# Kernel optimization log

Measured on AMD Instinct MI355X. Metric: run time of the kernel, lower is better.

## Reference

```python
import jax, jax.numpy as jnp
import numpy as np

N = 50000      # nodes
E = 800000     # edges (avg degree 16)
D_IN, D_H, D_OUT = 128, 256, 128


def setup_inputs() -> dict:
    key = jax.random.key(0)
    ks = jax.random.split(key, 8)
    x = jax.random.normal(ks[0], (N, D_IN), dtype=jnp.float32)
    edge_index = jax.random.randint(ks[1], (2, E), 0, N, dtype=jnp.int64)
    s1 = 1.0 / np.sqrt(D_IN).astype(np.float32)
    s2 = 1.0 / np.sqrt(D_H).astype(np.float32)
    return {
        "x": x,
        "edge_index": edge_index,
        "W1l": jax.random.normal(ks[2], (D_H, D_IN), jnp.float32) * s1,
        "b1l": jnp.zeros((D_H,), jnp.float32),
        "W1r": jax.random.normal(ks[3], (D_H, D_IN), jnp.float32) * s1,
        "W2l": jax.random.normal(ks[4], (D_OUT, D_H), jnp.float32) * s2,
        "b2l": jnp.zeros((D_OUT,), jnp.float32),
        "W2r": jax.random.normal(ks[5], (D_OUT, D_H), jnp.float32) * s2,
    }


def sage_conv(x, src, dst, Wl, bl, Wr):
    # mean-aggregate source features into destination nodes
    agg = jax.ops.segment_sum(x[src], dst, num_segments=N)           # [N, d_in]
    deg = jax.ops.segment_sum(jnp.ones((src.shape[0],), x.dtype), dst, num_segments=N)
    mean = agg / jnp.maximum(deg, 1.0)[:, None]
    # lin_l(mean_agg) + lin_r(x_root); lin_r has no bias (PyG SAGEConv default)
    return mean @ Wl.T + bl + x @ Wr.T


def reference(x, edge_index, W1l, b1l, W1r, W2l, b2l, W2r):
    src, dst = edge_index[0], edge_index[1]
    h = sage_conv(x, src, dst, W1l, b1l, W1r)
    h = jax.nn.relu(h)  # dropout inactive in eval mode
    return sage_conv(h, src, dst, W2l, b2l, W2r)
```

## Files before the change

### kernel.cpp

```cpp
#include <hip/hip_runtime.h>


typedef __attribute__((ext_vector_type(8))) short bf16x8;
typedef __attribute__((ext_vector_type(4))) float floatx4;

__device__ inline unsigned short f2b(float f) {
  unsigned int x = __float_as_uint(f);
  unsigned int r = (x + 0x7fffu + ((x >> 16) & 1u)) >> 16;
  return (unsigned short)r;
}
__device__ inline float blo(unsigned int u) { return __uint_as_float(u << 16); }
__device__ inline float bhi(unsigned int u) { return __uint_as_float(u & 0xffff0000u); }

#define ACC8(A, u)                                            \
  {                                                           \
    A[0] += blo((u).x); A[1] += bhi((u).x);                   \
    A[2] += blo((u).y); A[3] += bhi((u).y);                   \
    A[4] += blo((u).z); A[5] += bhi((u).z);                   \
    A[6] += blo((u).w); A[7] += bhi((u).w);                   \
  }

__global__ void prep_kernel(const float* __restrict__ x,
                            const float* __restrict__ W1l, const float* __restrict__ W1r,
                            const float* __restrict__ W2l, const float* __restrict__ W2r,
                            unsigned short* __restrict__ Wc1, unsigned short* __restrict__ Wc2,
                            unsigned short* __restrict__ A1,
                            int* __restrict__ cnt, int* __restrict__ off, int N, int E) {
  int i = blockIdx.x * blockDim.x + threadIdx.x;
  if (i < 65536) {
    int j = i >> 8, k = i & 255;
    float v1 = (k < 128) ? W1l[j * 128 + k] : W1r[j * 128 + (k - 128)];
    Wc1[i] = f2b(v1);
    float v2 = (j < 128) ? W2l[j * 256 + k] : W2r[(j - 128) * 256 + k];
    Wc2[i] = f2b(v2);
  }
  if (i < N) cnt[i] = 0;
  if (i == 0) off[N] = E;
  if (i < N * 32) {
    int n = i >> 5, c = (i & 31) * 4;
    float4 v = *(const float4*)(x + (size_t)n * 128 + c);
    uint2 p;
    p.x = (unsigned int)f2b(v.x) | ((unsigned int)f2b(v.y) << 16);
    p.y = (unsigned int)f2b(v.z) | ((unsigned int)f2b(v.w) << 16);
    *(uint2*)(A1 + (size_t)n * 256 + 128 + c) = p;
  }
}

__global__ void hist_kernel(const int* __restrict__ dst, int* __restrict__ cnt,
                            int* __restrict__ rank, int E) {
  int i = blockIdx.x * blockDim.x + threadIdx.x;
  int e = i * 4;
  if (e + 3 < E) {
    int4 d = *(const int4*)(dst + e);
    int4 r;
    r.x = atomicAdd(&cnt[d.x], 1);
    r.y = atomicAdd(&cnt[d.y], 1);
    r.z = atomicAdd(&cnt[d.z], 1);
    r.w = atomicAdd(&cnt[d.w], 1);
    *(int4*)(rank + e) = r;
  } else {
    for (; e < E; e++) rank[e] = atomicAdd(&cnt[dst[e]], 1);
  }
}

__global__ __launch_bounds__(1024) void scan_blocks_kernel(const int* __restrict__ cnt,
                                                           int* __restrict__ off,
                                                           int* __restrict__ bsum, int N) {
  __shared__ int wsum[16];
  __shared__ int wincl[16];
  const int tid = threadIdx.x;
  const int lane = tid & 63;
  const int wv = tid >> 6;
  const int i = blockIdx.x * 1024 + tid;
  const int v = (i < N) ? cnt[i] : 0;
  int s = v;
#pragma unroll
  for (int o = 1; o < 64; o <<= 1) {
    int t = __shfl_up(s, o, 64);
    if (lane >= o) s += t;
  }
  if (lane == 63) wsum[wv] = s;
  __syncthreads();
  if (tid < 16) {
    int ws = wsum[tid];
#pragma unroll
    for (int o = 1; o < 16; o <<= 1) {
      int t = __shfl_up(ws, o, 16);
      if ((tid & 15) >= o) ws += t;
    }
    wincl[tid] = ws;
  }
  __syncthreads();
  const int wo = wv ? wincl[wv - 1] : 0;
  if (i < N) off[i] = wo + s - v;
  if (tid == 1023) bsum[blockIdx.x] = wo + s;
}

__global__ __launch_bounds__(1024) void scan_add_kernel(int* __restrict__ off,
                                                        const int* __restrict__ bsum, int N, int SB) {
  __shared__ int bofs[64];
  const int tid = threadIdx.x;
  if (tid < 64) {
    int v = (tid < SB) ? bsum[tid] : 0;
    int s = v;
#pragma unroll
    for (int o = 1; o < 64; o <<= 1) {
      int t = __shfl_up(s, o, 64);
      if (tid >= o) s += t;
    }
    bofs[tid] = s - v;
  }
  __syncthreads();
  int i = blockIdx.x * 1024 + tid;
  if (i < N) off[i] = off[i] + bofs[blockIdx.x];
}

__global__ void fill_kernel(const int* __restrict__ src, const int* __restrict__ dst,
                            const int* __restrict__ rank, const int* __restrict__ off,
                            int* __restrict__ csr, int E) {
  int i = blockIdx.x * blockDim.x + threadIdx.x;
  int e = i * 4;
  if (e + 3 < E) {
    int4 d = *(const int4*)(dst + e);
    int4 r = *(const int4*)(rank + e);
    int4 s = *(const int4*)(src + e);
    csr[off[d.x] + r.x] = s.x;
    csr[off[d.y] + r.y] = s.y;
    csr[off[d.z] + r.z] = s.z;
    csr[off[d.w] + r.w] = s.w;
  } else {
    for (; e < E; e++) csr[off[dst[e]] + rank[e]] = src[e];
  }
}

__global__ void gather1_kernel(const unsigned short* __restrict__ feat,
                               const int* __restrict__ csr, const int* __restrict__ off,
                               unsigned short* __restrict__ ob, int N) {
  int wid = (blockIdx.x * blockDim.x + threadIdx.x) >> 6;
  if (wid >= N) return;
  const int lane = threadIdx.x & 63;
  const int slot = lane >> 3;
  const int j = lane & 7;
  const int c0 = j * 8;
  const int s0 = off[wid], s1 = off[wid + 1];
  float a[16] = {};
  int e = s0 + slot;
  for (; e + 8 < s1; e += 16) {
    int i0 = csr[e], i1 = csr[e + 8];
    uint4 u0 = *(const uint4*)(feat + (size_t)i0 * 256 + c0);
    uint4 v0 = *(const uint4*)(feat + (size_t)i0 * 256 + 64 + c0);
    uint4 u1 = *(const uint4*)(feat + (size_t)i1 * 256 + c0);
    uint4 v1 = *(const uint4*)(feat + (size_t)i1 * 256 + 64 + c0);
    ACC8(a, u0); ACC8((a + 8), v0);
    ACC8(a, u1); ACC8((a + 8), v1);
  }
  for (; e < s1; e += 8) {
    int i0 = csr[e];
    uint4 u0 = *(const uint4*)(feat + (size_t)i0 * 256 + c0);
    uint4 v0 = *(const uint4*)(feat + (size_t)i0 * 256 + 64 + c0);
    ACC8(a, u0); ACC8((a + 8), v0);
  }
#pragma unroll
  for (int k = 0; k < 16; k++) {
    a[k] += __shfl_xor(a[k], 8, 64);
    a[k] += __shfl_xor(a[k], 16, 64);
    a[k] += __shfl_xor(a[k], 32, 64);
  }
  if (slot == 0) {
    const float inv = 1.0f / fmaxf((float)(s1 - s0), 1.0f);
    uint4 p;
    p.x = (unsigned int)f2b(a[0] * inv) | ((unsigned int)f2b(a[1] * inv) << 16);
    p.y = (unsigned int)f2b(a[2] * inv) | ((unsigned int)f2b(a[3] * inv) << 16);
    p.z = (unsigned int)f2b(a[4] * inv) | ((unsigned int)f2b(a[5] * inv) << 16);
    p.w = (unsigned int)f2b(a[6] * inv) | ((unsigned int)f2b(a[7] * inv) << 16);
    *(uint4*)(ob + (size_t)wid * 256 + c0) = p;
    p.x = (unsigned int)f2b(a[8] * inv) | ((unsigned int)f2b(a[9] * inv) << 16);
    p.y = (unsigned int)f2b(a[10] * inv) | ((unsigned int)f2b(a[11] * inv) << 16);
    p.z = (unsigned int)f2b(a[12] * inv) | ((unsigned int)f2b(a[13] * inv) << 16);
    p.w = (unsigned int)f2b(a[14] * inv) | ((unsigned int)f2b(a[15] * inv) << 16);
    *(uint4*)(ob + (size_t)wid * 256 + 64 + c0) = p;
  }
}

__global__ void gather2_kernel(const unsigned short* __restrict__ t,
                               const int* __restrict__ csr, const int* __restrict__ off,
                               float* __restrict__ out, int N) {
  int wid = (blockIdx.x * blockDim.x + threadIdx.x) >> 6;
  if (wid >= N) return;
  const int lane = threadIdx.x & 63;
  const int slot = lane >> 3;
  const int j = lane & 7;
  const int c0 = j * 8;
  const int s0 = off[wid], s1 = off[wid + 1];
  float a[16] = {};
  int e = s0 + slot;
  for (; e + 8 < s1; e += 16) {
    int i0 = csr[e], i1 = csr[e + 8];
    uint4 u0 = *(const uint4*)(t + (size_t)i0 * 128 + c0);
    uint4 v0 = *(const uint4*)(t + (size_t)i0 * 128 + 64 + c0);
    uint4 u1 = *(const uint4*)(t + (size_t)i1 * 128 + c0);
    uint4 v1 = *(const uint4*)(t + (size_t)i1 * 128 + 64 + c0);
    ACC8(a, u0); ACC8((a + 8), v0);
    ACC8(a, u1); ACC8((a + 8), v1);
  }
  for (; e < s1; e += 8) {
    int i0 = csr[e];
    uint4 u0 = *(const uint4*)(t + (size_t)i0 * 128 + c0);
    uint4 v0 = *(const uint4*)(t + (size_t)i0 * 128 + 64 + c0);
    ACC8(a, u0); ACC8((a + 8), v0);
  }
#pragma unroll
  for (int k = 0; k < 16; k++) {
    a[k] += __shfl_xor(a[k], 8, 64);
    a[k] += __shfl_xor(a[k], 16, 64);
    a[k] += __shfl_xor(a[k], 32, 64);
  }
  if (slot == 0) {
    const float inv = 1.0f / fmaxf((float)(s1 - s0), 1.0f);
    float4* o0 = (float4*)(out + (size_t)wid * 128 + c0);
    float4* o1 = (float4*)(out + (size_t)wid * 128 + 64 + c0);
    float4 r0 = o0[0], r1 = o0[1], r2 = o1[0], r3 = o1[1];
    r0.x += a[0] * inv;  r0.y += a[1] * inv;  r0.z += a[2] * inv;  r0.w += a[3] * inv;
    r1.x += a[4] * inv;  r1.y += a[5] * inv;  r1.z += a[6] * inv;  r1.w += a[7] * inv;
    r2.x += a[8] * inv;  r2.y += a[9] * inv;  r2.z += a[10] * inv; r2.w += a[11] * inv;
    r3.x += a[12] * inv; r3.y += a[13] * inv; r3.z += a[14] * inv; r3.w += a[15] * inv;
    o0[0] = r0; o0[1] = r1; o1[0] = r2; o1[1] = r3;
  }
}

__global__ __launch_bounds__(256, 2)
void gemm_fused(const unsigned short* __restrict__ A,
                const unsigned short* __restrict__ Wc1,
                const unsigned short* __restrict__ Wc2,
                const float* __restrict__ b1, const float* __restrict__ b2,
                unsigned short* __restrict__ tb, float* __restrict__ out, int M) {
  constexpr int LDW = 72;
  constexpr int LDH = 264;
  __shared__ __align__(16) unsigned short Hs[64 * LDH];
  __shared__ __align__(16) unsigned short As[64 * LDW];
  __shared__ __align__(16) unsigned short Ws[256 * LDW];
  const int t = threadIdx.x;
  const int lane = t & 63;
  const int wave = t >> 6;
  const int wn = wave * 64;
  const int l15 = lane & 15;
  const int quad = lane >> 4;
  const int m_blk = blockIdx.x * 64;

  {
    floatx4 acc[4][4] = {};
    for (int kc = 0; kc < 256; kc += 64) {
      __syncthreads();
#pragma unroll
      for (int i = 0; i < 2; i++) {
        int c = t + 256 * i;
        int row = c >> 3, col = (c & 7) * 8;
        int ar = m_blk + row;
        if (ar >= M) ar = M - 1;
        *(uint4*)(As + row * LDW + col) = *(const uint4*)(A + (size_t)ar * 256 + kc + col);
      }
#pragma unroll
      for (int i = 0; i < 8; i++) {
        int c = t + 256 * i;
        int row = c >> 3, col = (c & 7) * 8;
        *(uint4*)(Ws + row * LDW + col) = *(const uint4*)(Wc1 + (size_t)row * 256 + kc + col);
      }
      __syncthreads();
#pragma unroll
      for (int ks = 0; ks < 64; ks += 32) {
        bf16x8 af[4], bfr[4];
#pragma unroll
        for (int mt = 0; mt < 4; mt++)
          af[mt] = *(const bf16x8*)(As + (mt * 16 + l15) * LDW + ks + quad * 8);
#pragma unroll
        for (int nt = 0; nt < 4; nt++)
          bfr[nt] = *(const bf16x8*)(Ws + (wn + nt * 16 + l15) * LDW + ks + quad * 8);
#pragma unroll
        for (int mt = 0; mt < 4; mt++)
#pragma unroll
          for (int nt = 0; nt < 4; nt++)
            acc[mt][nt] = __builtin_amdgcn_mfma_f32_16x16x32_bf16(af[mt], bfr[nt], acc[mt][nt], 0, 0, 0);
      }
    }
#pragma unroll
    for (int nt = 0; nt < 4; nt++) {
      const int jl = wn + nt * 16 + l15;
      const float bv = b1[jl];
#pragma unroll
      for (int mt = 0; mt < 4; mt++) {
#pragma unroll
        for (int r = 0; r < 4; r++) {
          const int row = mt * 16 + quad * 4 + r;
          Hs[row * LDH + jl] = f2b(fmaxf(acc[mt][nt][r] + bv, 0.f));
        }
      }
    }
  }

  {
    floatx4 acc[4][4] = {};
    for (int kc = 0; kc < 256; kc += 64) {
      __syncthreads();
#pragma unroll
      for (int i = 0; i < 8; i++) {
        int c = t + 256 * i;
        int row = c >> 3, col = (c & 7) * 8;
        *(uint4*)(Ws + row * LDW + col) = *(const uint4*)(Wc2 + (size_t)row * 256 + kc + col);
      }
      __syncthreads();
#pragma unroll
      for (int ks = 0; ks < 64; ks += 32) {
        bf16x8 af[4], bfr[4];
#pragma unroll
        for (int mt = 0; mt < 4; mt++)
          af[mt] = *(const bf16x8*)(Hs + (mt * 16 + l15) * LDH + kc + ks + quad * 8);
#pragma unroll
        for (int nt = 0; nt < 4; nt++)
          bfr[nt] = *(const bf16x8*)(Ws + (wn + nt * 16 + l15) * LDW + ks + quad * 8);
#pragma unroll
        for (int mt = 0; mt < 4; mt++)
#pragma unroll
          for (int nt = 0; nt < 4; nt++)
            acc[mt][nt] = __builtin_amdgcn_mfma_f32_16x16x32_bf16(af[mt], bfr[nt], acc[mt][nt], 0, 0, 0);
      }
    }
#pragma unroll
    for (int nt = 0; nt < 4; nt++) {
      const int j = wn + nt * 16 + l15;
#pragma unroll
      for (int mt = 0; mt < 4; mt++) {
#pragma unroll
        for (int r = 0; r < 4; r++) {
          const int node = m_blk + mt * 16 + quad * 4 + r;
          if (node >= M) continue;
          const float v = acc[mt][nt][r];
          if (j < 128) {
            tb[(size_t)node * 128 + j] = f2b(v);
          } else {
            out[(size_t)node * 128 + (j - 128)] = v + b2[j - 128];
          }
        }
      }
    }
  }
}

extern "C" void kernel_launch(void* const* d_in, const int* in_sizes, int n_in,
                              void* d_out, int out_size, void* d_ws, size_t ws_size,
                              hipStream_t stream) {
  const float* x   = (const float*)d_in[0];
  const int*  eidx = (const int*)d_in[1];
  const float* W1l = (const float*)d_in[2];
  const float* b1l = (const float*)d_in[3];
  const float* W1r = (const float*)d_in[4];
  const float* W2l = (const float*)d_in[5];
  const float* b2l = (const float*)d_in[6];
  const float* W2r = (const float*)d_in[7];
  float* out = (float*)d_out;

  const int N = in_sizes[0] / 128;
  const int E = in_sizes[1] / 2;
  const int* src = eidx;
  const int* dst = eidx + E;

  int* cnt  = (int*)d_ws;
  int* off  = cnt + N;
  int* bsum = off + N + 1;
  int* rank = bsum + 64;
  int* csr  = rank + E;
  size_t ioff = ((size_t)(N + N + 1 + 64 + 2 * E) * 4 + 15) & ~(size_t)15;
  unsigned short* A1  = (unsigned short*)((char*)d_ws + ioff);
  unsigned short* tb  = A1 + (size_t)N * 256;
  unsigned short* Wc1 = tb + (size_t)N * 128;
  unsigned short* Wc2 = Wc1 + 65536;

  const int SB = (N + 1023) / 1024;

  prep_kernel<<<(N * 32 + 255) / 256, 256, 0, stream>>>(x, W1l, W1r, W2l, W2r,
                                                        Wc1, Wc2, A1, cnt, off, N, E);
  hist_kernel<<<(E / 4 + 255) / 256, 256, 0, stream>>>(dst, cnt, rank, E);
  scan_blocks_kernel<<<SB, 1024, 0, stream>>>(cnt, off, bsum, N);
  scan_add_kernel<<<SB, 1024, 0, stream>>>(off, bsum, N, SB);
  fill_kernel<<<(E / 4 + 255) / 256, 256, 0, stream>>>(src, dst, rank, off, csr, E);

  const int gblocks = (N + 3) / 4;
  gather1_kernel<<<gblocks, 256, 0, stream>>>(A1 + 128, csr, off, A1, N);

  gemm_fused<<<(N + 63) / 64, 256, 0, stream>>>(A1, Wc1, Wc2, b1l, b2l, tb, out, N);

  gather2_kernel<<<gblocks, 256, 0, stream>>>(tb, csr, off, out, N);
}
```

Measured before the change: 272.9 us.

## Load GEMM operands directly from global memory, dropping LDS staging tiles

The fused two-layer GEMM kernel no longer stages A and weight tiles through shared memory. Each lane now reads its MFMA fragments straight from global memory (A/Wc1, then Hs/Wc2), which removes the per-chunk __syncthreads barriers. The launch bound is raised to 4 blocks per CU because LDS use drops to the Hs buffer alone. The trade-off is that fragment loads become strided 16-byte global reads, and weight rows are re-fetched by every block and wave, so the kernel relies on cache hits in place of LDS reuse. The tighter register budget may also cause spills.

After: 282.1 us. +3.4%, slower.

```diff
diff --git a/kernel.cpp b/kernel.cpp
--- a/kernel.cpp
+++ b/kernel.cpp
@@ -228,17 +228,14 @@
   }
 }
 
-__global__ __launch_bounds__(256, 2)
+__global__ __launch_bounds__(256, 4)
 void gemm_fused(const unsigned short* __restrict__ A,
                 const unsigned short* __restrict__ Wc1,
                 const unsigned short* __restrict__ Wc2,
                 const float* __restrict__ b1, const float* __restrict__ b2,
                 unsigned short* __restrict__ tb, float* __restrict__ out, int M) {
-  constexpr int LDW = 72;
   constexpr int LDH = 264;
   __shared__ __align__(16) unsigned short Hs[64 * LDH];
-  __shared__ __align__(16) unsigned short As[64 * LDW];
-  __shared__ __align__(16) unsigned short Ws[256 * LDW];
   const int t = threadIdx.x;
   const int lane = t & 63;
   const int wave = t >> 6;
@@ -247,98 +244,88 @@
   const int quad = lane >> 4;
   const int m_blk = blockIdx.x * 64;
 
-  {
-    floatx4 acc[4][4] = {};
-    for (int kc = 0; kc < 256; kc += 64) {
-      __syncthreads();
-#pragma unroll
-      for (int i = 0; i < 2; i++) {
-        int c = t + 256 * i;
-        int row = c >> 3, col = (c & 7) * 8;
-        int ar = m_blk + row;
-        if (ar >= M) ar = M - 1;
-        *(uint4*)(As + row * LDW + col) = *(const uint4*)(A + (size_t)ar * 256 + kc + col);
-      }
-#pragma unroll
-      for (int i = 0; i < 8; i++) {
-        int c = t + 256 * i;
-        int row = c >> 3, col = (c & 7) * 8;
-        *(uint4*)(Ws + row * LDW + col) = *(const uint4*)(Wc1 + (size_t)row * 256 + kc + col);
-      }
-      __syncthreads();
-#pragma unroll
-      for (int ks = 0; ks < 64; ks += 32) {
-        bf16x8 af[4], bfr[4];
-#pragma unroll
-        for (int mt = 0; mt < 4; mt++)
-          af[mt] = *(const bf16x8*)(As + (mt * 16 + l15) * LDW + ks + quad * 8);
-#pragma unroll
-        for (int nt = 0; nt < 4; nt++)
-          bfr[nt] = *(const bf16x8*)(Ws + (wn + nt * 16 + l15) * LDW + ks + quad * 8);
-#pragma unroll
-        for (int mt = 0; mt < 4; mt++)
-#pragma unroll
-          for (int nt = 0; nt < 4; nt++)
-            acc[mt][nt] = __builtin_amdgcn_mfma_f32_16x16x32_bf16(af[mt], bfr[nt], acc[mt][nt], 0, 0, 0);
+  const unsigned short* ap[4];
+  const unsigned short* wp[4];
+#pragma unroll
+  for (int mt = 0; mt < 4; mt++) {
+    int ar = m_blk + mt * 16 + l15;
+    if (ar >= M) ar = M - 1;
+    ap[mt] = A + (size_t)ar * 256 + quad * 8;
+  }
+#pragma unroll
+  for (int nt = 0; nt < 4; nt++)
+    wp[nt] = Wc1 + (size_t)(wn + nt * 16 + l15) * 256 + quad * 8;
+
+  floatx4 acc[4][4] = {};
+
+#pragma unroll 2
+  for (int ks = 0; ks < 256; ks += 32) {
+    bf16x8 af[4], bfr[4];
+#pragma unroll
+    for (int mt = 0; mt < 4; mt++) af[mt] = *(const bf16x8*)(ap[mt] + ks);
+#pragma unroll
+    for (int nt = 0; nt < 4; nt++) bfr[nt] = *(const bf16x8*)(wp[nt] + ks);
+#pragma unroll
+    for (int mt = 0; mt < 4; mt++)
+#pragma unroll
+      for (int nt = 0; nt < 4; nt++)
+        acc[mt][nt] = __builtin_amdgcn_mfma_f32_16x16x32_bf16(af[mt], bfr[nt], acc[mt][nt], 0, 0, 0);
+  }
+
+#pragma unroll
+  for (int nt = 0; nt < 4; nt++) {
+    const int jl = wn + nt * 16 + l15;
+    const float bv = b1[jl];
+#pragma unroll
+    for (int mt = 0; mt < 4; mt++) {
+#pragma unroll
+      for (int r = 0; r < 4; r++) {
+        const int row = mt * 16 + quad * 4 + r;
+        Hs[row * LDH + jl] = f2b(fmaxf(acc[mt][nt][r] + bv, 0.f));
       }
     }
-#pragma unroll
-    for (int nt = 0; nt < 4; nt++) {
-      const int jl = wn + nt * 16 + l15;
-      const float bv = b1[jl];
-#pragma unroll
-      for (int mt = 0; mt < 4; mt++) {
-#pragma unroll
-        for (int r = 0; r < 4; r++) {
-          const int row = mt * 16 + quad * 4 + r;
-          Hs[row * LDH + jl] = f2b(fmaxf(acc[mt][nt][r] + bv, 0.f));
-        }
-      }
-    }
-  }
-
-  {
-    floatx4 acc[4][4] = {};
-    for (int kc = 0; kc < 256; kc += 64) {
-      __syncthreads();
-#pragma unroll
-      for (int i = 0; i < 8; i++) {
-        int c = t + 256 * i;
-        int row = c >> 3, col = (c & 7) * 8;
-        *(uint4*)(Ws + row * LDW + col) = *(const uint4*)(Wc2 + (size_t)row * 256 + kc + col);
-      }
-      __syncthreads();
-#pragma unroll
-      for (int ks = 0; ks < 64; ks += 32) {
-        bf16x8 af[4], bfr[4];
-#pragma unroll
-        for (int mt = 0; mt < 4; mt++)
-          af[mt] = *(const bf16x8*)(Hs + (mt * 16 + l15) * LDH + kc + ks + quad * 8);
-#pragma unroll
-        for (int nt = 0; nt < 4; nt++)
-          bfr[nt] = *(const bf16x8*)(Ws + (wn + nt * 16 + l15) * LDW + ks + quad * 8);
-#pragma unroll
-        for (int mt = 0; mt < 4; mt++)
-#pragma unroll
-          for (int nt = 0; nt < 4; nt++)
-            acc[mt][nt] = __builtin_amdgcn_mfma_f32_16x16x32_bf16(af[mt], bfr[nt], acc[mt][nt], 0, 0, 0);
-      }
-    }
-#pragma unroll
-    for (int nt = 0; nt < 4; nt++) {
-      const int j = wn + nt * 16 + l15;
-#pragma unroll
-      for (int mt = 0; mt < 4; mt++) {
-#pragma unroll
-        for (int r = 0; r < 4; r++) {
-          const int node = m_blk + mt * 16 + quad * 4 + r;
-          if (node >= M) continue;
-          const float v = acc[mt][nt][r];
-          if (j < 128) {
-            tb[(size_t)node * 128 + j] = f2b(v);
-          } else {
-            out[(size_t)node * 128 + (j - 128)] = v + b2[j - 128];
-          }
+  }
+  __syncthreads();
+
+#pragma unroll
+  for (int mt = 0; mt < 4; mt++)
+#pragma unroll
+    for (int nt = 0; nt < 4; nt++)
+      acc[mt][nt] = (floatx4){0.f, 0.f, 0.f, 0.f};
+#pragma unroll
+  for (int nt = 0; nt < 4; nt++)
+    wp[nt] = Wc2 + (size_t)(wn + nt * 16 + l15) * 256 + quad * 8;
+  const unsigned short* hp0 = Hs + l15 * LDH + quad * 8;
+
+#pragma unroll 2
+  for (int ks = 0; ks < 256; ks += 32) {
+    bf16x8 af[4], bfr[4];
+#pragma unroll
+    for (int mt = 0; mt < 4; mt++)
+      af[mt] = *(const bf16x8*)(hp0 + mt * 16 * LDH + ks);
+#pragma unroll
+    for (int nt = 0; nt < 4; nt++) bfr[nt] = *(const bf16x8*)(wp[nt] + ks);
+#pragma unroll
+    for (int mt = 0; mt < 4; mt++)
+#pragma unroll
+      for (int nt = 0; nt < 4; nt++)
+        acc[mt][nt] = __builtin_amdgcn_mfma_f32_16x16x32_bf16(af[mt], bfr[nt], acc[mt][nt], 0, 0, 0);
+  }
+
+#pragma unroll
+  for (int nt = 0; nt < 4; nt++) {
+    const int j = wn + nt * 16 + l15;
+#pragma unroll
+    for (int mt = 0; mt < 4; mt++) {
+#pragma unroll
+      for (int r = 0; r < 4; r++) {
+        const int node = m_blk + mt * 16 + quad * 4 + r;
+        if (node >= M) continue;
+        const float v = acc[mt][nt][r];
+        if (j < 128) {
+          tb[(size_t)node * 128 + j] = f2b(v);
+        } else {
+          out[(size_t)node * 128 + (j - 128)] = v + b2[j - 128];
         }
       }
     }
```
